# Optimization experiments

Hardware: AMD Instinct MI355X
Metric: run time of the kernel (lower is better)

The kernel has to match this reference:

```python
import jax, jax.numpy as jnp
import numpy as np

B, L, D = 16, 4096, 512


def setup_inputs() -> dict:
    key = jax.random.key(0)
    ks = jax.random.split(key, 8)
    s = 1.0 / np.sqrt(D)
    x = jax.random.normal(ks[0], (B, L, D), dtype=jnp.float32)
    Wk = jax.random.normal(ks[1], (D, D), dtype=jnp.float32) * s
    Wq = jax.random.normal(ks[2], (D, D), dtype=jnp.float32) * s
    Wv = jax.random.normal(ks[3], (D, D), dtype=jnp.float32) * s
    bk = jnp.zeros((D,), jnp.float32)
    bq = jnp.zeros((D,), jnp.float32)
    bv = jnp.zeros((D,), jnp.float32)
    lens = jax.random.randint(ks[4], (B,), 1, L + 1, dtype=jnp.int32)
    return {"x": x, "Wk": Wk, "bk": bk, "Wq": Wq, "bq": bq,
            "Wv": Wv, "bv": bv, "lens": lens}


def reference(x, Wk, bk, Wq, bq, Wv, bv, lens):
    # Dropout is identity in eval mode.
    x_k = jnp.tanh(jnp.einsum('bld,ed->ble', x, Wk) + bk)  # [B,L,D]
    x_q = jnp.tanh(jnp.einsum('bld,ed->ble', x, Wq) + bq)
    x_v = jnp.tanh(jnp.einsum('bld,ed->ble', x, Wv) + bv)
    # sum_j (x_k_i . x_q_j) == x_k_i . sum_j x_q_j  (algebraic collapse of the L x L bmm)
    q_sum = x_q.sum(axis=1)                                # [B,D]
    w = jnp.einsum('bld,bd->bl', x_k, q_sum) / (D ** 0.5)  # [B,L]
    pad = jnp.arange(L)[None, :] >= lens[:, None]          # True at padding
    w = jnp.where(pad, -jnp.inf, w)
    w = jax.nn.softmax(w, axis=1)                          # [B,L]
    # (x_v * w[...,None]).sum(-1) == x_v.sum(-1) * w
    return x_v.sum(axis=-1) * w                            # [B,L]
```

## Files before the change

### kernel.cpp

```cpp
#include <hip/hip_runtime.h>
#include <hip/hip_bf16.h>

typedef __attribute__((ext_vector_type(4)))  int   i32x4;
typedef __attribute__((ext_vector_type(16))) int   i32x16;
typedef __attribute__((ext_vector_type(16))) float f32x16;
typedef __attribute__((ext_vector_type(8)))  short short8;

#define SC1 (1.0f/4096.0f)
#define SC2 (1.0f/524288.0f)

static __device__ __forceinline__ float ftanh(float x) {
  float e = __builtin_amdgcn_exp2f(x * 2.885390081777927f);
  return 1.0f - 2.0f * __builtin_amdgcn_rcpf(e + 1.0f);
}
static __device__ __forceinline__ unsigned short bf16_rn(float f) {
  unsigned u = __float_as_uint(f);
  u += 0x7FFFu + ((u >> 16) & 1u);
  return (unsigned short)(u >> 16);
}
static __device__ __forceinline__ void quant2(float x, float sc, float inv, float losc,
                                              int& hi, int& lo) {
  float t  = __builtin_fmaf(x, sc, 12582912.0f);
  hi = __float_as_int(t) - 0x4B400000;
  float hf = t - 12582912.0f;
  float r  = __builtin_fmaf(hf, -inv, x);
  float t2 = __builtin_fmaf(r, losc, 12582912.0f);
  lo = __float_as_int(t2) - 0x4B400000;
}
static __device__ __forceinline__ void gll16(const void* g, void* l) {
  __builtin_amdgcn_global_load_lds((const __attribute__((address_space(1))) unsigned int*)g,
                                   (__attribute__((address_space(3))) unsigned int*)l, 16, 0, 0);
}
#define MFMA_I8(ACC, A, B) \
  asm("v_mfma_i32_32x32x32_i8 %0, %1, %2, %0" : "+v"(ACC) : "v"(A), "v"(B))

__global__ void prep_w(const float* __restrict__ Wq, const float* __restrict__ Wk,
                       const float* __restrict__ Wv,
                       char* __restrict__ B1, char* __restrict__ B2) {
  int gid = blockIdx.x * 256 + threadIdx.x;
  if (gid < 65536) {
    int chunk = gid >> 12, g = gid & 4095;
    char* dst = B1 + chunk * 65536 + g * 16;
    if (g < 2048) {
      int sel = g >> 10;
      int gg = g & 1023, nt = gg >> 6, lane = gg & 63;
      const float* src = Wq + (size_t)(nt * 32 + (lane & 31)) * 512 + chunk * 32 + (lane >> 5) * 16;
      union { char b[16]; i32x4 v; } ob;
#pragma unroll
      for (int j = 0; j < 16; ++j) {
        int h, l; quant2(src[j], 256.f, 1.f / 256.f, 32768.f, h, l);
        ob.b[j] = (char)(sel ? l : h);
      }
      *(i32x4*)dst = ob.v;
    } else {
      int gg = g - 2048, nt = gg >> 7, ks = (gg >> 6) & 1, lane = gg & 63;
      const float* src = Wv + (size_t)(nt * 32 + (lane & 31)) * 512 + chunk * 32 + ks * 16 + (lane >> 5) * 8;
      union { unsigned short s[8]; i32x4 v; } ob;
#pragma unroll
      for (int j = 0; j < 8; ++j) ob.s[j] = bf16_rn(src[j]);
      *(i32x4*)dst = ob.v;
    }
  } else {
    int gid2 = gid - 65536;
    int chunk = gid2 >> 11, g = gid2 & 2047;
    char* dst = B2 + chunk * 32768 + g * 16;
    int sel = g >> 10, gg = g & 1023, nt = gg >> 6, lane = gg & 63;
    const float* src = Wk + (size_t)(nt * 32 + (lane & 31)) * 512 + chunk * 32 + (lane >> 5) * 16;
    union { char b[16]; i32x4 v; } ob;
#pragma unroll
    for (int j = 0; j < 16; ++j) {
      int h, l; quant2(src[j], 256.f, 1.f / 256.f, 32768.f, h, l);
      ob.b[j] = (char)(sel ? l : h);
    }
    *(i32x4*)dst = ob.v;
  }
}

static __device__ __forceinline__ void stageAi8(char* Ab, int row, int d0, float4 xv) {
  const int mt = row >> 5, l31 = row & 31;
  int h0, l0, h1, l1, h2, l2, h3, l3;
  quant2(xv.x, 16.f, 0.0625f, 2048.f, h0, l0);
  quant2(xv.y, 16.f, 0.0625f, 2048.f, h1, l1);
  quant2(xv.z, 16.f, 0.0625f, 2048.f, h2, l2);
  quant2(xv.w, 16.f, 0.0625f, 2048.f, h3, l3);
  unsigned wh = (h0 & 255) | ((h1 & 255) << 8) | ((h2 & 255) << 16) | ((unsigned)(h3 & 255) << 24);
  unsigned wl = (l0 & 255) | ((l1 & 255) << 8) | ((l2 & 255) << 16) | ((unsigned)(l3 & 255) << 24);
  const int lane8 = (d0 >> 4) * 32 + l31, j = d0 & 15;
  *(unsigned*)(Ab + (mt * 64 + lane8) * 16 + j) = wh;
  *(unsigned*)(Ab + 2048 + (mt * 64 + lane8) * 16 + j) = wl;
}
static __device__ __forceinline__ void stageAv(char* Ab, int row, int d0, float4 xv) {
  const int mt = row >> 5, l31 = row & 31;
  unsigned long long b0 = bf16_rn(xv.x), b1 = bf16_rn(xv.y), b2 = bf16_rn(xv.z), b3 = bf16_rn(xv.w);
  unsigned long long vv = b0 | (b1 << 16) | (b2 << 32) | (b3 << 48);
  const int ks = d0 >> 4, rem = d0 & 15, hs8 = rem >> 3, j8 = rem & 7;
  *(unsigned long long*)(Ab + ((mt * 2 + ks) * 64 + hs8 * 32 + l31) * 16 + j8 * 2) = vv;
}

__global__ __launch_bounds__(1024, 4) void pass_q(
    const float* __restrict__ x, const char* __restrict__ B1,
    const float* __restrict__ bq, float* __restrict__ qpart) {
  extern __shared__ char smem[];
  char* Bb0 = smem;          char* Bb1 = smem + 32768;
  char* Ab0 = smem + 65536;  char* Ab1 = smem + 69632;
  float* redq = (float*)(smem + 73728);

  const int tid = threadIdx.x, lane = tid & 63, w = tid >> 6;
  const int l31 = lane & 31;
  const int mt = w >> 3, ng = w & 7;
  const int tile = blockIdx.x;
  const int stag = tile & 15;
  const int row = tid >> 3, d0 = (tid & 7) * 4;
  const float* gxr = x + ((size_t)tile * 64 + row) * 512 + d0;

  i32x16 q1[2] = {}, q2[2] = {};
  float4 xcur = {};

  if (tid < 512) { xcur = *(const float4*)(gxr + stag * 32); stageAi8(Ab0, row, d0, xcur); }
  {
    const char* src = B1 + (size_t)stag * 65536 + tid * 16;
    gll16(src, Bb0 + tid * 16);
    gll16(src + 16384, Bb0 + 16384 + tid * 16);
  }
  if (tid < 512) xcur = *(const float4*)(gxr + (((stag + 1) & 15)) * 32);

#pragma unroll 1
  for (int c = 0; c < 16; ++c) {
    const int p = c & 1;
    char* Bc = p ? Bb1 : Bb0;  char* Bn = p ? Bb0 : Bb1;
    char* Ac = p ? Ab1 : Ab0;  char* An = p ? Ab0 : Ab1;
    __syncthreads();
    if (c < 15) {
      const char* src = B1 + (size_t)(((c + 1 + stag) & 15)) * 65536 + tid * 16;
      gll16(src, Bn + tid * 16);
      gll16(src + 16384, Bn + 16384 + tid * 16);
    }
    float4 xnext = xcur;
    if (tid < 512) {
      if (c < 14) xnext = *(const float4*)(gxr + (((c + 2 + stag) & 15)) * 32);
      if (c < 15) stageAi8(An, row, d0, xcur);
    }

    const int lo16 = lane * 16;
    i32x4 ah = *(const i32x4*)(Ac + mt * 1024 + lo16);
    i32x4 al = *(const i32x4*)(Ac + 2048 + mt * 1024 + lo16);
#pragma unroll
    for (int nn = 0; nn < 2; ++nn) {
      const int nt = ng * 2 + nn;
      i32x4 bh = *(const i32x4*)(Bc + nt * 1024 + lo16);
      i32x4 bl = *(const i32x4*)(Bc + 16384 + nt * 1024 + lo16);
      MFMA_I8(q1[nn], ah, bh);
      MFMA_I8(q2[nn], ah, bl);
      MFMA_I8(q2[nn], al, bh);
    }
    xcur = xnext;
  }

#pragma unroll
  for (int nn = 0; nn < 2; ++nn) {
    const int col = (ng * 2 + nn) * 32 + l31;
    const float bc = bq[col];
    float cs = 0.f;
#pragma unroll
    for (int r = 0; r < 16; ++r)
      cs += ftanh(__builtin_fmaf((float)q1[nn][r], SC1,
                  __builtin_fmaf((float)q2[nn][r], SC2, bc)));
    cs += __shfl_xor(cs, 32);
    if (lane < 32) redq[mt * 512 + col] = cs;
  }
  __syncthreads();
  if (tid < 512) qpart[(size_t)tile * 512 + tid] = redq[tid] + redq[512 + tid];
}

__global__ __launch_bounds__(1024, 4) void pass_v(
    const float* __restrict__ x, const char* __restrict__ B1,
    const float* __restrict__ bv, float* __restrict__ svout) {
  extern __shared__ char smem[];
  char* Bb0 = smem;          char* Bb1 = smem + 32768;
  char* Ab0 = smem + 65536;  char* Ab1 = smem + 69632;
  float* redv = (float*)(smem + 73728);

  const int tid = threadIdx.x, lane = tid & 63, w = tid >> 6;
  const int l31 = lane & 31, hs = lane >> 5;
  const int mt = w >> 3, ng = w & 7;
  const int tile = blockIdx.x;
  const int stag = tile & 15;
  const int row = tid >> 3, d0 = (tid & 7) * 4;
  const float* gxr = x + ((size_t)tile * 64 + row) * 512 + d0;

  f32x16 accv[2] = {};
  float4 xcur = {};

  if (tid < 512) { xcur = *(const float4*)(gxr + stag * 32); stageAv(Ab0, row, d0, xcur); }
  {
    const char* src = B1 + (size_t)stag * 65536 + 32768 + tid * 16;
    gll16(src, Bb0 + tid * 16);
    gll16(src + 16384, Bb0 + 16384 + tid * 16);
  }
  if (tid < 512) xcur = *(const float4*)(gxr + (((stag + 1) & 15)) * 32);

#pragma unroll 1
  for (int c = 0; c < 16; ++c) {
    const int p = c & 1;
    char* Bc = p ? Bb1 : Bb0;  char* Bn = p ? Bb0 : Bb1;
    char* Ac = p ? Ab1 : Ab0;  char* An = p ? Ab0 : Ab1;
    __syncthreads();
    if (c < 15) {
      const char* src = B1 + (size_t)(((c + 1 + stag) & 15)) * 65536 + 32768 + tid * 16;
      gll16(src, Bn + tid * 16);
      gll16(src + 16384, Bn + 16384 + tid * 16);
    }
    float4 xnext = xcur;
    if (tid < 512) {
      if (c < 14) xnext = *(const float4*)(gxr + (((c + 2 + stag) & 15)) * 32);
      if (c < 15) stageAv(An, row, d0, xcur);
    }

    const int lo16 = lane * 16;
#pragma unroll
    for (int ks = 0; ks < 2; ++ks) {
      short8 av = *(const short8*)(Ac + (mt * 2 + ks) * 1024 + lo16);
#pragma unroll
      for (int nn = 0; nn < 2; ++nn) {
        const int nt = ng * 2 + nn;
        short8 bvf = *(const short8*)(Bc + (nt * 2 + ks) * 1024 + lo16);
        accv[nn] = __builtin_amdgcn_mfma_f32_32x32x16_bf16(av, bvf, accv[nn], 0, 0, 0);
      }
    }
    xcur = xnext;
  }

  const float bv0 = bv[(ng * 2 + 0) * 32 + l31];
  const float bv1 = bv[(ng * 2 + 1) * 32 + l31];
  __syncthreads();
#pragma unroll
  for (int r = 0; r < 16; ++r) {
    float s = ftanh(accv[0][r] + bv0) + ftanh(accv[1][r] + bv1);
#pragma unroll
    for (int off = 1; off <= 16; off <<= 1) s += __shfl_xor(s, off);
    if (l31 == 0) redv[ng * 64 + mt * 32 + (r & 3) + 8 * (r >> 2) + 4 * hs] = s;
  }
  __syncthreads();
  if (tid < 64) {
    float s = 0.f;
#pragma unroll
    for (int j = 0; j < 8; ++j) s += redv[j * 64 + tid];
    svout[(size_t)tile * 64 + tid] = s;
  }
}

__global__ __launch_bounds__(1024, 4) void pass_k(
    const float* __restrict__ x, const char* __restrict__ B2,
    const float* __restrict__ bk, const float* __restrict__ q_sum,
    float* __restrict__ scores) {
  extern __shared__ char smem[];
  char* Bb0 = smem;          char* Bb1 = smem + 32768;
  char* Ab0 = smem + 65536;  char* Ab1 = smem + 69632;
  float* redk = (float*)(smem + 73728);

  const int tid = threadIdx.x, lane = tid & 63, w = tid >> 6;
  const int l31 = lane & 31, hs = lane >> 5;
  const int mt = w >> 3, ng = w & 7;
  const int tile = blockIdx.x;
  const int stag = tile & 15;
  const int row = tid >> 3, d0 = (tid & 7) * 4;
  const float* gxr = x + ((size_t)tile * 64 + row) * 512 + d0;

  i32x16 k1[2] = {}, k2[2] = {};
  float4 xcur = {};

  if (tid < 512) { xcur = *(const float4*)(gxr + stag * 32); stageAi8(Ab0, row, d0, xcur); }
  {
    const char* src = B2 + (size_t)stag * 32768 + tid * 16;
    gll16(src, Bb0 + tid * 16);
    gll16(src + 16384, Bb0 + 16384 + tid * 16);
  }
  if (tid < 512) xcur = *(const float4*)(gxr + (((stag + 1) & 15)) * 32);

#pragma unroll 1
  for (int c = 0; c < 16; ++c) {
    const int p = c & 1;
    char* Bc = p ? Bb1 : Bb0;  char* Bn = p ? Bb0 : Bb1;
    char* Ac = p ? Ab1 : Ab0;  char* An = p ? Ab0 : Ab1;
    __syncthreads();
    if (c < 15) {
      const char* src = B2 + (size_t)(((c + 1 + stag) & 15)) * 32768 + tid * 16;
      gll16(src, Bn + tid * 16);
      gll16(src + 16384, Bn + 16384 + tid * 16);
    }
    float4 xnext = xcur;
    if (tid < 512) {
      if (c < 14) xnext = *(const float4*)(gxr + (((c + 2 + stag) & 15)) * 32);
      if (c < 15) stageAi8(An, row, d0, xcur);
    }

    const int lo16 = lane * 16;
    i32x4 ah = *(const i32x4*)(Ac + mt * 1024 + lo16);
    i32x4 al = *(const i32x4*)(Ac + 2048 + mt * 1024 + lo16);
#pragma unroll
    for (int nn = 0; nn < 2; ++nn) {
      const int nt = ng * 2 + nn;
      i32x4 bh = *(const i32x4*)(Bc + nt * 1024 + lo16);
      i32x4 bl = *(const i32x4*)(Bc + 16384 + nt * 1024 + lo16);
      MFMA_I8(k1[nn], ah, bh);
      MFMA_I8(k2[nn], ah, bl);
      MFMA_I8(k2[nn], al, bh);
    }
    xcur = xnext;
  }

  const int b = tile >> 6;
  const int c0 = (ng * 2 + 0) * 32 + l31, c1 = (ng * 2 + 1) * 32 + l31;
  const float qs0 = q_sum[b * 512 + c0], qs1 = q_sum[b * 512 + c1];
  const float bk0 = bk[c0], bk1 = bk[c1];
  __syncthreads();
#pragma unroll
  for (int r = 0; r < 16; ++r) {
    float p0 = __builtin_fmaf((float)k1[0][r], SC1,
               __builtin_fmaf((float)k2[0][r], SC2, bk0));
    float p1 = __builtin_fmaf((float)k1[1][r], SC1,
               __builtin_fmaf((float)k2[1][r], SC2, bk1));
    float s = ftanh(p0) * qs0 + ftanh(p1) * qs1;
#pragma unroll
    for (int off = 1; off <= 16; off <<= 1) s += __shfl_xor(s, off);
    if (l31 == 0) redk[ng * 64 + mt * 32 + (r & 3) + 8 * (r >> 2) + 4 * hs] = s;
  }
  __syncthreads();
  if (tid < 64) {
    float s = 0.f;
#pragma unroll
    for (int j = 0; j < 8; ++j) s += redk[j * 64 + tid];
    scores[(size_t)tile * 64 + tid] = s;
  }
}

__global__ void reduce_q(const float* __restrict__ qpart, float* __restrict__ q_sum) {
  int b = blockIdx.x, e = threadIdx.x;
  const float* p = qpart + (size_t)b * 64 * 512 + e;
  float s = 0.f;
#pragma unroll 4
  for (int j = 0; j < 64; ++j) s += p[j * 512];
  q_sum[b * 512 + e] = s;
}

__global__ void softmax_out(const float* __restrict__ scores,
                            const float* __restrict__ sv,
                            const int* __restrict__ lens,
                            float* __restrict__ out) {
  const int b = blockIdx.x, tid = threadIdx.x;
  const int lane = tid & 63, wid = tid >> 6;
  const int len = lens[b];
  const float scale = 0.04419417382415922f;
  __shared__ float sb[4], sb2[4];

  float sreg[16];
  const float* sc = scores + (size_t)b * 4096;
#pragma unroll
  for (int j = 0; j < 16; ++j) sreg[j] = sc[tid + j * 256] * scale;

  float m = -1e30f;
#pragma unroll
  for (int j = 0; j < 16; ++j)
    if (tid + j * 256 < len) m = fmaxf(m, sreg[j]);
#pragma unroll
  for (int off = 32; off >= 1; off >>= 1) m = fmaxf(m, __shfl_xor(m, off));
  if (lane == 0) sb[wid] = m;
  __syncthreads();
  m = fmaxf(fmaxf(sb[0], sb[1]), fmaxf(sb[2], sb[3]));

  float s = 0.f;
#pragma unroll
  for (int j = 0; j < 16; ++j)
    if (tid + j * 256 < len) s += expf(sreg[j] - m);
#pragma unroll
  for (int off = 32; off >= 1; off >>= 1) s += __shfl_xor(s, off);
  if (lane == 0) sb2[wid] = s;
  __syncthreads();
  const float inv = 1.f / (sb2[0] + sb2[1] + sb2[2] + sb2[3]);

  const float* svb = sv + (size_t)b * 4096;
  float* ob = out + (size_t)b * 4096;
#pragma unroll
  for (int j = 0; j < 16; ++j) {
    int l = tid + j * 256;
    ob[l] = (l < len) ? svb[l] * expf(sreg[j] - m) * inv : 0.0f;
  }
}

extern "C" void kernel_launch(void* const* d_in, const int* in_sizes, int n_in,
                              void* d_out, int out_size, void* d_ws, size_t ws_size,
                              hipStream_t stream) {
  const float* x  = (const float*)d_in[0];
  const float* Wk = (const float*)d_in[1];
  const float* bk = (const float*)d_in[2];
  const float* Wq = (const float*)d_in[3];
  const float* bq = (const float*)d_in[4];
  const float* Wv = (const float*)d_in[5];
  const float* bv = (const float*)d_in[6];
  const int* lens = (const int*)d_in[7];
  float* out = (float*)d_out;

  char* ws = (char*)d_ws;
  char*  B1     = ws;
  char*  B2     = ws + 1048576;
  float* qpart  = (float*)(ws + 1572864);
  float* q_sum  = (float*)(ws + 3670016);
  float* svbuf  = (float*)(ws + 3702784);
  float* scores = (float*)(ws + 3964928);

  prep_w<<<384, 256, 0, stream>>>(Wq, Wk, Wv, B1, B2);
  pass_q<<<1024, 1024, 77824, stream>>>(x, B1, bq, qpart);
  pass_v<<<1024, 1024, 75776, stream>>>(x, B1, bv, svbuf);
  reduce_q<<<16, 512, 0, stream>>>(qpart, q_sum);
  pass_k<<<1024, 1024, 75776, stream>>>(x, B2, bk, q_sum, scores);
  softmax_out<<<16, 256, 0, stream>>>(scores, svbuf, lens, out);
}
```

Before: 235.3 us.

## Double K-chunk per pipeline stage to halve barriers in Q/V/K GEMM passes

Each loop iteration in pass_q, pass_v and pass_k now stages two 32-wide K chunks (64 of K) into doubled LDS buffers and runs both sub-chunks' MFMAs, so the loop runs 8 times instead of 16. The aim is to halve the number of barriers and loop-overhead points per tile. The one-iteration-ahead register prefetch of x is removed; x is now loaded and staged in the same iteration, behind an explicit full vmcnt/lgkmcnt drain before each barrier. LDS per block grows to about 148 KB, which likely allows only one 1024-thread block per CU and exposes more global-load latency.

After: 228.5 us. -2.9%, faster.

```diff
diff --git a/kernel.cpp b/kernel.cpp
--- a/kernel.cpp
+++ b/kernel.cpp
@@ -8,6 +8,11 @@
 
 #define SC1 (1.0f/4096.0f)
 #define SC2 (1.0f/524288.0f)
+
+#define DRAIN_SYNC() do { \
+    asm volatile("s_waitcnt vmcnt(0) lgkmcnt(0)" ::: "memory"); \
+    __syncthreads(); \
+  } while (0)
 
 static __device__ __forceinline__ float ftanh(float x) {
   float e = __builtin_amdgcn_exp2f(x * 2.885390081777927f);
@@ -101,59 +106,74 @@
     const float* __restrict__ x, const char* __restrict__ B1,
     const float* __restrict__ bq, float* __restrict__ qpart) {
   extern __shared__ char smem[];
-  char* Bb0 = smem;          char* Bb1 = smem + 32768;
-  char* Ab0 = smem + 65536;  char* Ab1 = smem + 69632;
-  float* redq = (float*)(smem + 73728);
+  char* Bb0 = smem;            char* Bb1 = smem + 65536;
+  char* Ab0 = smem + 131072;   char* Ab1 = smem + 139264;
+  float* redq = (float*)(smem + 147456);
 
   const int tid = threadIdx.x, lane = tid & 63, w = tid >> 6;
   const int l31 = lane & 31;
   const int mt = w >> 3, ng = w & 7;
   const int tile = blockIdx.x;
-  const int stag = tile & 15;
+  const int stag = tile & 7;
   const int row = tid >> 3, d0 = (tid & 7) * 4;
   const float* gxr = x + ((size_t)tile * 64 + row) * 512 + d0;
 
   i32x16 q1[2] = {}, q2[2] = {};
-  float4 xcur = {};
-
-  if (tid < 512) { xcur = *(const float4*)(gxr + stag * 32); stageAi8(Ab0, row, d0, xcur); }
+
+  if (tid < 512) {
+    float4 xa = *(const float4*)(gxr + (2 * stag) * 32);
+    float4 xb = *(const float4*)(gxr + (2 * stag + 1) * 32);
+    stageAi8(Ab0, row, d0, xa);
+    stageAi8(Ab0 + 4096, row, d0, xb);
+  }
   {
-    const char* src = B1 + (size_t)stag * 65536 + tid * 16;
-    gll16(src, Bb0 + tid * 16);
-    gll16(src + 16384, Bb0 + 16384 + tid * 16);
-  }
-  if (tid < 512) xcur = *(const float4*)(gxr + (((stag + 1) & 15)) * 32);
+    const char* s0 = B1 + (size_t)(2 * stag) * 65536 + tid * 16;
+    const char* s1 = B1 + (size_t)(2 * stag + 1) * 65536 + tid * 16;
+    gll16(s0, Bb0 + tid * 16);
+    gll16(s0 + 16384, Bb0 + 16384 + tid * 16);
+    gll16(s1, Bb0 + 32768 + tid * 16);
+    gll16(s1 + 16384, Bb0 + 49152 + tid * 16);
+  }
 
 #pragma unroll 1
-  for (int c = 0; c < 16; ++c) {
-    const int p = c & 1;
+  for (int i = 0; i < 8; ++i) {
+    const int p = i & 1;
     char* Bc = p ? Bb1 : Bb0;  char* Bn = p ? Bb0 : Bb1;
     char* Ac = p ? Ab1 : Ab0;  char* An = p ? Ab0 : Ab1;
-    __syncthreads();
-    if (c < 15) {
-      const char* src = B1 + (size_t)(((c + 1 + stag) & 15)) * 65536 + tid * 16;
-      gll16(src, Bn + tid * 16);
-      gll16(src + 16384, Bn + 16384 + tid * 16);
-    }
-    float4 xnext = xcur;
-    if (tid < 512) {
-      if (c < 14) xnext = *(const float4*)(gxr + (((c + 2 + stag) & 15)) * 32);
-      if (c < 15) stageAi8(An, row, d0, xcur);
+    DRAIN_SYNC();
+    const int ni = (i + 1 + stag) & 7;
+    if (i < 7) {
+      const char* s0 = B1 + (size_t)(2 * ni) * 65536 + tid * 16;
+      const char* s1 = B1 + (size_t)(2 * ni + 1) * 65536 + tid * 16;
+      gll16(s0, Bn + tid * 16);
+      gll16(s0 + 16384, Bn + 16384 + tid * 16);
+      gll16(s1, Bn + 32768 + tid * 16);
+      gll16(s1 + 16384, Bn + 49152 + tid * 16);
+    }
+    if (tid < 512 && i < 7) {
+      float4 xa = *(const float4*)(gxr + (2 * ni) * 32);
+      float4 xb = *(const float4*)(gxr + (2 * ni + 1) * 32);
+      stageAi8(An, row, d0, xa);
+      stageAi8(An + 4096, row, d0, xb);
     }
 
     const int lo16 = lane * 16;
-    i32x4 ah = *(const i32x4*)(Ac + mt * 1024 + lo16);
-    i32x4 al = *(const i32x4*)(Ac + 2048 + mt * 1024 + lo16);
-#pragma unroll
-    for (int nn = 0; nn < 2; ++nn) {
-      const int nt = ng * 2 + nn;
-      i32x4 bh = *(const i32x4*)(Bc + nt * 1024 + lo16);
-      i32x4 bl = *(const i32x4*)(Bc + 16384 + nt * 1024 + lo16);
-      MFMA_I8(q1[nn], ah, bh);
-      MFMA_I8(q2[nn], ah, bl);
-      MFMA_I8(q2[nn], al, bh);
-    }
-    xcur = xnext;
+#pragma unroll
+    for (int sub = 0; sub < 2; ++sub) {
+      const char* Ap = Ac + sub * 4096;
+      const char* Bp = Bc + sub * 32768;
+      i32x4 ah = *(const i32x4*)(Ap + mt * 1024 + lo16);
+      i32x4 al = *(const i32x4*)(Ap + 2048 + mt * 1024 + lo16);
+#pragma unroll
+      for (int nn = 0; nn < 2; ++nn) {
+        const int nt = ng * 2 + nn;
+        i32x4 bh = *(const i32x4*)(Bp + nt * 1024 + lo16);
+        i32x4 bl = *(const i32x4*)(Bp + 16384 + nt * 1024 + lo16);
+        MFMA_I8(q1[nn], ah, bh);
+        MFMA_I8(q2[nn], ah, bl);
+        MFMA_I8(q2[nn], al, bh);
+      }
+    }
   }
 
 #pragma unroll
@@ -176,58 +196,73 @@
     const float* __restrict__ x, const char* __restrict__ B1,
     const float* __restrict__ bv, float* __restrict__ svout) {
   extern __shared__ char smem[];
-  char* Bb0 = smem;          char* Bb1 = smem + 32768;
-  char* Ab0 = smem + 65536;  char* Ab1 = smem + 69632;
-  float* redv = (float*)(smem + 73728);
+  char* Bb0 = smem;            char* Bb1 = smem + 65536;
+  char* Ab0 = smem + 131072;   char* Ab1 = smem + 139264;
+  float* redv = (float*)(smem + 147456);
 
   const int tid = threadIdx.x, lane = tid & 63, w = tid >> 6;
   const int l31 = lane & 31, hs = lane >> 5;
   const int mt = w >> 3, ng = w & 7;
   const int tile = blockIdx.x;
-  const int stag = tile & 15;
+  const int stag = tile & 7;
   const int row = tid >> 3, d0 = (tid & 7) * 4;
   const float* gxr = x + ((size_t)tile * 64 + row) * 512 + d0;
 
   f32x16 accv[2] = {};
-  float4 xcur = {};
-
-  if (tid < 512) { xcur = *(const float4*)(gxr + stag * 32); stageAv(Ab0, row, d0, xcur); }
+
+  if (tid < 512) {
+    float4 xa = *(const float4*)(gxr + (2 * stag) * 32);
+    float4 xb = *(const float4*)(gxr + (2 * stag + 1) * 32);
+    stageAv(Ab0, row, d0, xa);
+    stageAv(Ab0 + 4096, row, d0, xb);
+  }
   {
-    const char* src = B1 + (size_t)stag * 65536 + 32768 + tid * 16;
-    gll16(src, Bb0 + tid * 16);
-    gll16(src + 16384, Bb0 + 16384 + tid * 16);
-  }
-  if (tid < 512) xcur = *(const float4*)(gxr + (((stag + 1) & 15)) * 32);
+    const char* s0 = B1 + (size_t)(2 * stag) * 65536 + 32768 + tid * 16;
+    const char* s1 = B1 + (size_t)(2 * stag + 1) * 65536 + 32768 + tid * 16;
+    gll16(s0, Bb0 + tid * 16);
+    gll16(s0 + 16384, Bb0 + 16384 + tid * 16);
+    gll16(s1, Bb0 + 32768 + tid * 16);
+    gll16(s1 + 16384, Bb0 + 49152 + tid * 16);
+  }
 
 #pragma unroll 1
-  for (int c = 0; c < 16; ++c) {
-    const int p = c & 1;
+  for (int i = 0; i < 8; ++i) {
+    const int p = i & 1;
     char* Bc = p ? Bb1 : Bb0;  char* Bn = p ? Bb0 : Bb1;
     char* Ac = p ? Ab1 : Ab0;  char* An = p ? Ab0 : Ab1;
-    __syncthreads();
-    if (c < 15) {
-      const char* src = B1 + (size_t)(((c + 1 + stag) & 15)) * 65536 + 32768 + tid * 16;
-      gll16(src, Bn + tid * 16);
-      gll16(src + 16384, Bn + 16384 + tid * 16);
-    }
-    float4 xnext = xcur;
-    if (tid < 512) {
-      if (c < 14) xnext = *(const float4*)(gxr + (((c + 2 + stag) & 15)) * 32);
-      if (c < 15) stageAv(An, row, d0, xcur);
+    DRAIN_SYNC();
+    const int ni = (i + 1 + stag) & 7;
+    if (i < 7) {
+      const char* s0 = B1 + (size_t)(2 * ni) * 65536 + 32768 + tid * 16;
+      const char* s1 = B1 + (size_t)(2 * ni + 1) * 65536 + 32768 + tid * 16;
+      gll16(s0, Bn + tid * 16);
+      gll16(s0 + 16384, Bn + 16384 + tid * 16);
+      gll16(s1, Bn + 32768 + tid * 16);
+      gll16(s1 + 16384, Bn + 49152 + tid * 16);
+    }
+    if (tid < 512 && i < 7) {
+      float4 xa = *(const float4*)(gxr + (2 * ni) * 32);
+      float4 xb = *(const float4*)(gxr + (2 * ni + 1) * 32);
+      stageAv(An, row, d0, xa);
+      stageAv(An + 4096, row, d0, xb);
     }
 
     const int lo16 = lane * 16;
 #pragma unroll
-    for (int ks = 0; ks < 2; ++ks) {
-      short8 av = *(const short8*)(Ac + (mt * 2 + ks) * 1024 + lo16);
-#pragma unroll
-      for (int nn = 0; nn < 2; ++nn) {
-        const int nt = ng * 2 + nn;
-        short8 bvf = *(const short8*)(Bc + (nt * 2 + ks) * 1024 + lo16);
-        accv[nn] = __builtin_amdgcn_mfma_f32_32x32x16_bf16(av, bvf, accv[nn], 0, 0, 0);
+    for (int sub = 0; sub < 2; ++sub) {
+      const char* Ap = Ac + sub * 4096;
+      const char* Bp = Bc + sub * 32768;
+#pragma unroll
+      for (int ks = 0; ks < 2; ++ks) {
+        short8 av = *(const short8*)(Ap + (mt * 2 + ks) * 1024 + lo16);
+#pragma unroll
+        for (int nn = 0; nn < 2; ++nn) {
+          const int nt = ng * 2 + nn;
+          short8 bvf = *(const short8*)(Bp + (nt * 2 + ks) * 1024 + lo16);
+          accv[nn] = __builtin_amdgcn_mfma_f32_32x32x16_bf16(av, bvf, accv[nn], 0, 0, 0);
+        }
       }
     }
-    xcur = xnext;
   }
 
   const float bv0 = bv[(ng * 2 + 0) * 32 + l31];
@@ -254,59 +289,74 @@
     const float* __restrict__ bk, const float* __restrict__ q_sum,
     float* __restrict__ scores) {
   extern __shared__ char smem[];
-  char* Bb0 = smem;          char* Bb1 = smem + 32768;
-  char* Ab0 = smem + 65536;  char* Ab1 = smem + 69632;
-  float* redk = (float*)(smem + 73728);
+  char* Bb0 = smem;            char* Bb1 = smem + 65536;
+  char* Ab0 = smem + 131072;   char* Ab1 = smem + 139264;
+  float* redk = (float*)(smem + 147456);
 
   const int tid = threadIdx.x, lane = tid & 63, w = tid >> 6;
   const int l31 = lane & 31, hs = lane >> 5;
   const int mt = w >> 3, ng = w & 7;
   const int tile = blockIdx.x;
-  const int stag = tile & 15;
+  const int stag = tile & 7;
   const int row = tid >> 3, d0 = (tid & 7) * 4;
   const float* gxr = x + ((size_t)tile * 64 + row) * 512 + d0;
 
   i32x16 k1[2] = {}, k2[2] = {};
-  float4 xcur = {};
-
-  if (tid < 512) { xcur = *(const float4*)(gxr + stag * 32); stageAi8(Ab0, row, d0, xcur); }
+
+  if (tid < 512) {
+    float4 xa = *(const float4*)(gxr + (2 * stag) * 32);
+    float4 xb = *(const float4*)(gxr + (2 * stag + 1) * 32);
+    stageAi8(Ab0, row, d0, xa);
+    stageAi8(Ab0 + 4096, row, d0, xb);
+  }
   {
-    const char* src = B2 + (size_t)stag * 32768 + tid * 16;
-    gll16(src, Bb0 + tid * 16);
-    gll16(src + 16384, Bb0 + 16384 + tid * 16);
-  }
-  if (tid < 512) xcur = *(const float4*)(gxr + (((stag + 1) & 15)) * 32);
+    const char* s0 = B2 + (size_t)(2 * stag) * 32768 + tid * 16;
+    const char* s1 = B2 + (size_t)(2 * stag + 1) * 32768 + tid * 16;
+    gll16(s0, Bb0 + tid * 16);
+    gll16(s0 + 16384, Bb0 + 16384 + tid * 16);
+    gll16(s1, Bb0 + 32768 + tid * 16);
+    gll16(s1 + 16384, Bb0 + 49152 + tid * 16);
+  }
 
 #pragma unroll 1
-  for (int c = 0; c < 16; ++c) {
-    const int p = c & 1;
+  for (int i = 0; i < 8; ++i) {
+    const int p = i & 1;
     char* Bc = p ? Bb1 : Bb0;  char* Bn = p ? Bb0 : Bb1;
     char* Ac = p ? Ab1 : Ab0;  char* An = p ? Ab0 : Ab1;
-    __syncthreads();
-    if (c < 15) {
-      const char* src = B2 + (size_t)(((c + 1 + stag) & 15)) * 32768 + tid * 16;
-      gll16(src, Bn + tid * 16);
-      gll16(src + 16384, Bn + 16384 + tid * 16);
-    }
-    float4 xnext = xcur;
-    if (tid < 512) {
-      if (c < 14) xnext = *(const float4*)(gxr + (((c + 2 + stag) & 15)) * 32);
-      if (c < 15) stageAi8(An, row, d0, xcur);
+    DRAIN_SYNC();
+    const int ni = (i + 1 + stag) & 7;
+    if (i < 7) {
+      const char* s0 = B2 + (size_t)(2 * ni) * 32768 + tid * 16;
+      const char* s1 = B2 + (size_t)(2 * ni + 1) * 32768 + tid * 16;
+      gll16(s0, Bn + tid * 16);
+      gll16(s0 + 16384, Bn + 16384 + tid * 16);
+      gll16(s1, Bn + 32768 + tid * 16);
+      gll16(s1 + 16384, Bn + 49152 + tid * 16);
+    }
+    if (tid < 512 && i < 7) {
+      float4 xa = *(const float4*)(gxr + (2 * ni) * 32);
+      float4 xb = *(const float4*)(gxr + (2 * ni + 1) * 32);
+      stageAi8(An, row, d0, xa);
+      stageAi8(An + 4096, row, d0, xb);
     }
 
     const int lo16 = lane * 16;
-    i32x4 ah = *(const i32x4*)(Ac + mt * 1024 + lo16);
-    i32x4 al = *(const i32x4*)(Ac + 2048 + mt * 1024 + lo16);
-#pragma unroll
-    for (int nn = 0; nn < 2; ++nn) {
-      const int nt = ng * 2 + nn;
-      i32x4 bh = *(const i32x4*)(Bc + nt * 1024 + lo16);
-      i32x4 bl = *(const i32x4*)(Bc + 16384 + nt * 1024 + lo16);
-      MFMA_I8(k1[nn], ah, bh);
-      MFMA_I8(k2[nn], ah, bl);
-      MFMA_I8(k2[nn], al, bh);
-    }
-    xcur = xnext;
+#pragma unroll
+    for (int sub = 0; sub < 2; ++sub) {
+      const char* Ap = Ac + sub * 4096;
+      const char* Bp = Bc + sub * 32768;
+      i32x4 ah = *(const i32x4*)(Ap + mt * 1024 + lo16);
+      i32x4 al = *(const i32x4*)(Ap + 2048 + mt * 1024 + lo16);
+#pragma unroll
+      for (int nn = 0; nn < 2; ++nn) {
+        const int nt = ng * 2 + nn;
+        i32x4 bh = *(const i32x4*)(Bp + nt * 1024 + lo16);
+        i32x4 bl = *(const i32x4*)(Bp + 16384 + nt * 1024 + lo16);
+        MFMA_I8(k1[nn], ah, bh);
+        MFMA_I8(k2[nn], ah, bl);
+        MFMA_I8(k2[nn], al, bh);
+      }
+    }
   }
 
   const int b = tile >> 6;
@@ -409,9 +459,9 @@
   float* scores = (float*)(ws + 3964928);
 
   prep_w<<<384, 256, 0, stream>>>(Wq, Wk, Wv, B1, B2);
-  pass_q<<<1024, 1024, 77824, stream>>>(x, B1, bq, qpart);
-  pass_v<<<1024, 1024, 75776, stream>>>(x, B1, bv, svbuf);
+  pass_q<<<1024, 1024, 151552, stream>>>(x, B1, bq, qpart);
+  pass_v<<<1024, 1024, 149504, stream>>>(x, B1, bv, svbuf);
   reduce_q<<<16, 512, 0, stream>>>(qpart, q_sum);
-  pass_k<<<1024, 1024, 75776, stream>>>(x, B2, bk, q_sum, scores);
+  pass_k<<<1024, 1024, 149504, stream>>>(x, B2, bk, q_sum, scores);
   softmax_out<<<16, 256, 0, stream>>>(scores, svbuf, lens, out);
 }
```

## Triple-buffer weight tiles with partial vmcnt waits in projection passes

Applied to the files above, without the earlier changes.

Replaces the double-buffered B weight tiles in pass_q, pass_v and pass_k with a three-slot ring buffer. Loads are issued two chunks ahead, and `__syncthreads` becomes an explicit `s_waitcnt vmcnt(2)` plus `s_barrier`, with sched_barrier fences, so the newest prefetch can stay in flight across the barrier. The goal is to hide global-to-LDS latency for the weight tiles. In exchange, LDS per block grows from about 76KB to about 110KB, which may cut the number of resident blocks per CU.

Result: no change. 231.1 us (-1.8%).

```diff
diff --git a/kernel.cpp b/kernel.cpp
--- a/kernel.cpp
+++ b/kernel.cpp
@@ -8,6 +8,8 @@
 
 #define SC1 (1.0f/4096.0f)
 #define SC2 (1.0f/524288.0f)
+
+#define SBAR() __builtin_amdgcn_sched_barrier(0)
 
 static __device__ __forceinline__ float ftanh(float x) {
   float e = __builtin_amdgcn_exp2f(x * 2.885390081777927f);
@@ -97,13 +99,22 @@
   *(unsigned long long*)(Ab + ((mt * 2 + ks) * 64 + hs8 * 32 + l31) * 16 + j8 * 2) = vv;
 }
 
+#define PIPE_WAIT(LAST)                                                     \
+  do {                                                                      \
+    if (LAST) asm volatile("s_waitcnt vmcnt(0) lgkmcnt(0)" ::: "memory");   \
+    else      asm volatile("s_waitcnt vmcnt(2) lgkmcnt(0)" ::: "memory");   \
+    SBAR();                                                                 \
+    __builtin_amdgcn_s_barrier();                                           \
+    SBAR();                                                                 \
+  } while (0)
+
 __global__ __launch_bounds__(1024, 4) void pass_q(
     const float* __restrict__ x, const char* __restrict__ B1,
     const float* __restrict__ bq, float* __restrict__ qpart) {
   extern __shared__ char smem[];
-  char* Bb0 = smem;          char* Bb1 = smem + 32768;
-  char* Ab0 = smem + 65536;  char* Ab1 = smem + 69632;
-  float* redq = (float*)(smem + 73728);
+  char* Bb  = smem;
+  char* Ab0 = smem + 98304;  char* Ab1 = smem + 102400;
+  float* redq = (float*)(smem + 106496);
 
   const int tid = threadIdx.x, lane = tid & 63, w = tid >> 6;
   const int l31 = lane & 31;
@@ -116,31 +127,43 @@
   i32x16 q1[2] = {}, q2[2] = {};
   float4 xcur = {};
 
-  if (tid < 512) { xcur = *(const float4*)(gxr + stag * 32); stageAi8(Ab0, row, d0, xcur); }
-  {
-    const char* src = B1 + (size_t)stag * 65536 + tid * 16;
-    gll16(src, Bb0 + tid * 16);
-    gll16(src + 16384, Bb0 + 16384 + tid * 16);
-  }
+  if (tid < 512) {
+    float4 x0 = *(const float4*)(gxr + stag * 32);
+    stageAi8(Ab0, row, d0, x0);
+  }
+  SBAR();
+  {
+    const char* s = B1 + (size_t)stag * 65536 + tid * 16;
+    gll16(s, Bb + tid * 16);
+    gll16(s + 16384, Bb + 16384 + tid * 16);
+  }
+  SBAR();
   if (tid < 512) xcur = *(const float4*)(gxr + (((stag + 1) & 15)) * 32);
+  SBAR();
+  {
+    const char* s = B1 + (size_t)((stag + 1) & 15) * 65536 + tid * 16;
+    gll16(s, Bb + 32768 + tid * 16);
+    gll16(s + 16384, Bb + 32768 + 16384 + tid * 16);
+  }
 
 #pragma unroll 1
   for (int c = 0; c < 16; ++c) {
-    const int p = c & 1;
-    char* Bc = p ? Bb1 : Bb0;  char* Bn = p ? Bb0 : Bb1;
-    char* Ac = p ? Ab1 : Ab0;  char* An = p ? Ab0 : Ab1;
-    __syncthreads();
-    if (c < 15) {
-      const char* src = B1 + (size_t)(((c + 1 + stag) & 15)) * 65536 + tid * 16;
-      gll16(src, Bn + tid * 16);
-      gll16(src + 16384, Bn + 16384 + tid * 16);
-    }
-    float4 xnext = xcur;
-    if (tid < 512) {
-      if (c < 14) xnext = *(const float4*)(gxr + (((c + 2 + stag) & 15)) * 32);
-      if (c < 15) stageAi8(An, row, d0, xcur);
-    }
-
+    PIPE_WAIT(c == 15);
+    float4 xnew = xcur;
+    if (c < 14) {
+      const int cc2 = (c + 2 + stag) & 15;
+      if (tid < 512) xnew = *(const float4*)(gxr + cc2 * 32);
+      SBAR();
+      const char* s = B1 + (size_t)cc2 * 65536 + tid * 16;
+      char* dstB = Bb + ((c + 2) % 3) * 32768;
+      gll16(s, dstB + tid * 16);
+      gll16(s + 16384, dstB + 16384 + tid * 16);
+      SBAR();
+    }
+    if (c < 15 && tid < 512) stageAi8((c & 1) ? Ab0 : Ab1, row, d0, xcur);
+
+    const char* Ac = (c & 1) ? Ab1 : Ab0;
+    const char* Bc = Bb + (c % 3) * 32768;
     const int lo16 = lane * 16;
     i32x4 ah = *(const i32x4*)(Ac + mt * 1024 + lo16);
     i32x4 al = *(const i32x4*)(Ac + 2048 + mt * 1024 + lo16);
@@ -153,7 +176,7 @@
       MFMA_I8(q2[nn], ah, bl);
       MFMA_I8(q2[nn], al, bh);
     }
-    xcur = xnext;
+    xcur = xnew;
   }
 
 #pragma unroll
@@ -176,9 +199,9 @@
     const float* __restrict__ x, const char* __restrict__ B1,
     const float* __restrict__ bv, float* __restrict__ svout) {
   extern __shared__ char smem[];
-  char* Bb0 = smem;          char* Bb1 = smem + 32768;
-  char* Ab0 = smem + 65536;  char* Ab1 = smem + 69632;
-  float* redv = (float*)(smem + 73728);
+  char* Bb  = smem;
+  char* Ab0 = smem + 98304;  char* Ab1 = smem + 102400;
+  float* redv = (float*)(smem + 106496);
 
   const int tid = threadIdx.x, lane = tid & 63, w = tid >> 6;
   const int l31 = lane & 31, hs = lane >> 5;
@@ -191,31 +214,43 @@
   f32x16 accv[2] = {};
   float4 xcur = {};
 
-  if (tid < 512) { xcur = *(const float4*)(gxr + stag * 32); stageAv(Ab0, row, d0, xcur); }
-  {
-    const char* src = B1 + (size_t)stag * 65536 + 32768 + tid * 16;
-    gll16(src, Bb0 + tid * 16);
-    gll16(src + 16384, Bb0 + 16384 + tid * 16);
-  }
+  if (tid < 512) {
+    float4 x0 = *(const float4*)(gxr + stag * 32);
+    stageAv(Ab0, row, d0, x0);
+  }
+  SBAR();
+  {
+    const char* s = B1 + (size_t)stag * 65536 + 32768 + tid * 16;
+    gll16(s, Bb + tid * 16);
+    gll16(s + 16384, Bb + 16384 + tid * 16);
+  }
+  SBAR();
   if (tid < 512) xcur = *(const float4*)(gxr + (((stag + 1) & 15)) * 32);
+  SBAR();
+  {
+    const char* s = B1 + (size_t)((stag + 1) & 15) * 65536 + 32768 + tid * 16;
+    gll16(s, Bb + 32768 + tid * 16);
+    gll16(s + 16384, Bb + 32768 + 16384 + tid * 16);
+  }
 
 #pragma unroll 1
   for (int c = 0; c < 16; ++c) {
-    const int p = c & 1;
-    char* Bc = p ? Bb1 : Bb0;  char* Bn = p ? Bb0 : Bb1;
-    char* Ac = p ? Ab1 : Ab0;  char* An = p ? Ab0 : Ab1;
-    __syncthreads();
-    if (c < 15) {
-      const char* src = B1 + (size_t)(((c + 1 + stag) & 15)) * 65536 + 32768 + tid * 16;
-      gll16(src, Bn + tid * 16);
-      gll16(src + 16384, Bn + 16384 + tid * 16);
-    }
-    float4 xnext = xcur;
-    if (tid < 512) {
-      if (c < 14) xnext = *(const float4*)(gxr + (((c + 2 + stag) & 15)) * 32);
-      if (c < 15) stageAv(An, row, d0, xcur);
-    }
-
+    PIPE_WAIT(c == 15);
+    float4 xnew = xcur;
+    if (c < 14) {
+      const int cc2 = (c + 2 + stag) & 15;
+      if (tid < 512) xnew = *(const float4*)(gxr + cc2 * 32);
+      SBAR();
+      const char* s = B1 + (size_t)cc2 * 65536 + 32768 + tid * 16;
+      char* dstB = Bb + ((c + 2) % 3) * 32768;
+      gll16(s, dstB + tid * 16);
+      gll16(s + 16384, dstB + 16384 + tid * 16);
+      SBAR();
+    }
+    if (c < 15 && tid < 512) stageAv((c & 1) ? Ab0 : Ab1, row, d0, xcur);
+
+    const char* Ac = (c & 1) ? Ab1 : Ab0;
+    const char* Bc = Bb + (c % 3) * 32768;
     const int lo16 = lane * 16;
 #pragma unroll
     for (int ks = 0; ks < 2; ++ks) {
@@ -227,7 +262,7 @@
         accv[nn] = __builtin_amdgcn_mfma_f32_32x32x16_bf16(av, bvf, accv[nn], 0, 0, 0);
       }
     }
-    xcur = xnext;
+    xcur = xnew;
   }
 
   const float bv0 = bv[(ng * 2 + 0) * 32 + l31];
@@ -254,9 +289,9 @@
     const float* __restrict__ bk, const float* __restrict__ q_sum,
     float* __restrict__ scores) {
   extern __shared__ char smem[];
-  char* Bb0 = smem;          char* Bb1 = smem + 32768;
-  char* Ab0 = smem + 65536;  char* Ab1 = smem + 69632;
-  float* redk = (float*)(smem + 73728);
+  char* Bb  = smem;
+  char* Ab0 = smem + 98304;  char* Ab1 = smem + 102400;
+  float* redk = (float*)(smem + 106496);
 
   const int tid = threadIdx.x, lane = tid & 63, w = tid >> 6;
   const int l31 = lane & 31, hs = lane >> 5;
@@ -269,31 +304,43 @@
   i32x16 k1[2] = {}, k2[2] = {};
   float4 xcur = {};
 
-  if (tid < 512) { xcur = *(const float4*)(gxr + stag * 32); stageAi8(Ab0, row, d0, xcur); }
-  {
-    const char* src = B2 + (size_t)stag * 32768 + tid * 16;
-    gll16(src, Bb0 + tid * 16);
-    gll16(src + 16384, Bb0 + 16384 + tid * 16);
-  }
+  if (tid < 512) {
+    float4 x0 = *(const float4*)(gxr + stag * 32);
+    stageAi8(Ab0, row, d0, x0);
+  }
+  SBAR();
+  {
+    const char* s = B2 + (size_t)stag * 32768 + tid * 16;
+    gll16(s, Bb + tid * 16);
+    gll16(s + 16384, Bb + 16384 + tid * 16);
+  }
+  SBAR();
   if (tid < 512) xcur = *(const float4*)(gxr + (((stag + 1) & 15)) * 32);
+  SBAR();
+  {
+    const char* s = B2 + (size_t)((stag + 1) & 15) * 32768 + tid * 16;
+    gll16(s, Bb + 32768 + tid * 16);
+    gll16(s + 16384, Bb + 32768 + 16384 + tid * 16);
+  }
 
 #pragma unroll 1
   for (int c = 0; c < 16; ++c) {
-    const int p = c & 1;
-    char* Bc = p ? Bb1 : Bb0;  char* Bn = p ? Bb0 : Bb1;
-    char* Ac = p ? Ab1 : Ab0;  char* An = p ? Ab0 : Ab1;
-    __syncthreads();
-    if (c < 15) {
-      const char* src = B2 + (size_t)(((c + 1 + stag) & 15)) * 32768 + tid * 16;
-      gll16(src, Bn + tid * 16);
-      gll16(src + 16384, Bn + 16384 + tid * 16);
-    }
-    float4 xnext = xcur;
-    if (tid < 512) {
-      if (c < 14) xnext = *(const float4*)(gxr + (((c + 2 + stag) & 15)) * 32);
-      if (c < 15) stageAi8(An, row, d0, xcur);
-    }
-
+    PIPE_WAIT(c == 15);
+    float4 xnew = xcur;
+    if (c < 14) {
+      const int cc2 = (c + 2 + stag) & 15;
+      if (tid < 512) xnew = *(const float4*)(gxr + cc2 * 32);
+      SBAR();
+      const char* s = B2 + (size_t)cc2 * 32768 + tid * 16;
+      char* dstB = Bb + ((c + 2) % 3) * 32768;
+      gll16(s, dstB + tid * 16);
+      gll16(s + 16384, dstB + 16384 + tid * 16);
+      SBAR();
+    }
+    if (c < 15 && tid < 512) stageAi8((c & 1) ? Ab0 : Ab1, row, d0, xcur);
+
+    const char* Ac = (c & 1) ? Ab1 : Ab0;
+    const char* Bc = Bb + (c % 3) * 32768;
     const int lo16 = lane * 16;
     i32x4 ah = *(const i32x4*)(Ac + mt * 1024 + lo16);
     i32x4 al = *(const i32x4*)(Ac + 2048 + mt * 1024 + lo16);
@@ -306,7 +353,7 @@
       MFMA_I8(k2[nn], ah, bl);
       MFMA_I8(k2[nn], al, bh);
     }
-    xcur = xnext;
+    xcur = xnew;
   }
 
   const int b = tile >> 6;
@@ -409,9 +456,9 @@
   float* scores = (float*)(ws + 3964928);
 
   prep_w<<<384, 256, 0, stream>>>(Wq, Wk, Wv, B1, B2);
-  pass_q<<<1024, 1024, 77824, stream>>>(x, B1, bq, qpart);
-  pass_v<<<1024, 1024, 75776, stream>>>(x, B1, bv, svbuf);
+  pass_q<<<1024, 1024, 110592, stream>>>(x, B1, bq, qpart);
+  pass_v<<<1024, 1024, 108544, stream>>>(x, B1, bv, svbuf);
   reduce_q<<<16, 512, 0, stream>>>(qpart, q_sum);
-  pass_k<<<1024, 1024, 75776, stream>>>(x, B2, bk, q_sum, scores);
+  pass_k<<<1024, 1024, 108544, stream>>>(x, B2, bk, q_sum, scores);
   softmax_out<<<16, 256, 0, stream>>>(scores, svbuf, lens, out);
 }
```
